# Optimization experiments

Measured on AMD Instinct MI355X. Metric: run time of the kernel, lower is better.

## Reference

```python
import jax, jax.numpy as jnp
import numpy as np

H = 16      # query heads
G = 4       # kv heads
D = 64      # head dim
ROPE_BASE = 10000.0

def _rotate_half(t):
    t1, t2 = jnp.split(t, 2, axis=-1)
    return jnp.concatenate([-t2, t1], axis=-1)

def _rope_emb(n):
    inv_freq = 1.0 / (ROPE_BASE ** (jnp.arange(0, D, 2, dtype=jnp.float32) / D))
    freqs = jnp.outer(jnp.arange(n, dtype=jnp.float32), inv_freq)  # [n, D/2]
    return jnp.concatenate([freqs, freqs], axis=-1)               # [n, D]

def setup_inputs() -> dict:
    key = jax.random.key(0)
    k1, k2, k3, k4 = jax.random.split(key, 4)
    B, N, C = 2, 2048, 1024
    x = jax.random.normal(k1, (B, N, C), dtype=jnp.float32)
    w_q = jax.random.normal(k2, (C, C), dtype=jnp.float32) * 0.02
    w_kv = jax.random.normal(k3, (C, 2 * G * D), dtype=jnp.float32) * 0.02
    w_out = jax.random.normal(k4, (C, C), dtype=jnp.float32) * 0.02
    return {"x": x, "w_q": w_q, "w_kv": w_kv, "w_out": w_out}

def reference(x, w_q, w_kv, w_out):
    B, N, C = x.shape
    scale = D ** -0.5
    q = (x @ w_q).reshape(B, N, H, D).transpose(0, 2, 1, 3)        # [B,H,N,D]
    kv = x @ w_kv
    k, v = jnp.split(kv, 2, axis=-1)
    k = k.reshape(B, N, G, D).transpose(0, 2, 1, 3)                # [B,G,N,D]
    v = v.reshape(B, N, G, D).transpose(0, 2, 1, 3)
    emb = _rope_emb(N)                                             # [N,D]
    cos, sin = jnp.cos(emb), jnp.sin(emb)
    q = q * cos + _rotate_half(q) * sin
    k = k * cos + _rotate_half(k) * sin
    # NOTE: faithful to source einsum -- kv-head axis g is SUMMED (absent from output)
    scores = jnp.einsum('bhid,bgjd->bhij', q, k) * scale           # [B,H,N,N]
    probs = jax.nn.softmax(scores, axis=-1)
    out = jnp.einsum('bhij,bgjd->bhid', probs, v)                  # [B,H,N,D]
    out = out.transpose(0, 2, 1, 3).reshape(B, N, H * D)
    return out @ w_out
```

## Files before the change

### kernel.cpp

```cpp
#include <hip/hip_runtime.h>
#include <hip/hip_bf16.h>
#include <math.h>

#define B_ 2
#define N_ 2048
#define C_ 1024
#define H_ 16
#define G_ 4
#define D_ 64

using short8  = __attribute__((ext_vector_type(8))) short;
using float4v = __attribute__((ext_vector_type(4))) float;

__device__ __forceinline__ ushort f2bf(float f) {
    union { float f; unsigned u; } v; v.f = f;
    unsigned r = (v.u + 0x7FFF + ((v.u >> 16) & 1)) >> 16;
    return (ushort)r;
}
__device__ __forceinline__ float bf2f(ushort u) {
    union { unsigned u; float f; } t; t.u = ((unsigned)u) << 16; return t.f;
}
__device__ __forceinline__ unsigned pack_bf16(float a, float b) {
#if __has_builtin(__builtin_amdgcn_cvt_pk_bf16_f32)
    auto t = __builtin_amdgcn_cvt_pk_bf16_f32(a, b);
    unsigned r; __builtin_memcpy(&r, &t, 4); return r;
#else
    return (unsigned)f2bf(a) | ((unsigned)f2bf(b) << 16);
#endif
}
__device__ __forceinline__ float fexp2(float x) {
#if __has_builtin(__builtin_amdgcn_exp2f)
    return __builtin_amdgcn_exp2f(x);
#else
    return exp2f(x);
#endif
}

__global__ void convert_x(const float* __restrict__ x, ushort* __restrict__ xb) {
    int i = (blockIdx.x * 256 + threadIdx.x) * 4;
    float4 v = *(const float4*)(x + i);
    ushort4 o;
    o.x = f2bf(v.x); o.y = f2bf(v.y); o.z = f2bf(v.z); o.w = f2bf(v.w);
    *(ushort4*)(xb + i) = o;
}

__global__ void tconv(const float* __restrict__ src, ushort* __restrict__ dst,
                      int K, int N) {
    __shared__ float T[64][65];
    const int n0 = blockIdx.x * 64, k0 = blockIdx.y * 64;
    const int tid = threadIdx.x;
    #pragma unroll
    for (int s = 0; s < 16; ++s) {
        int idx = tid + s * 256; int r = idx >> 6, cc = idx & 63;
        T[r][cc] = src[(size_t)(k0 + r) * N + n0 + cc];
    }
    __syncthreads();
    #pragma unroll
    for (int s = 0; s < 16; ++s) {
        int idx = tid + s * 256; int r = idx >> 6, cc = idx & 63;
        dst[(size_t)(n0 + r) * K + k0 + cc] = f2bf(T[cc][r]);
    }
}

template <bool F32OUT>
__global__ __launch_bounds__(256) void gemm64(const ushort* __restrict__ A,
                                              const ushort* __restrict__ Bt,
                                              void* __restrict__ Cv,
                                              int M, int N, int K) {
    __shared__ __align__(16) ushort As[64 * 32];
    __shared__ __align__(16) ushort Bs[64 * 32];

    const int tid = threadIdx.x, wave = tid >> 6, lane = tid & 63;
    const int g = lane >> 4, c = lane & 15;
    const int wr = wave >> 1, wc = wave & 1;
    const int m0 = blockIdx.y * 64, n0 = blockIdx.x * 64;

    const int srow = wave * 16 + (lane >> 2), schunk = (lane & 3) * 8;
    const ushort* pa = A  + (size_t)(m0 + srow) * K + schunk;
    const ushort* pb = Bt + (size_t)(n0 + srow) * K + schunk;
    ushort* ldsA = &As[wave * 16 * 32];
    ushort* ldsB = &Bs[wave * 16 * 32];

    float4v acc[2][2] = {{{0,0,0,0},{0,0,0,0}},{{0,0,0,0},{0,0,0,0}}};

    for (int k0 = 0; k0 < K; k0 += 32) {
        __builtin_amdgcn_global_load_lds(
            (const __attribute__((address_space(1))) void*)(pa + k0),
            (__attribute__((address_space(3))) void*)ldsA, 16, 0, 0);
        __builtin_amdgcn_global_load_lds(
            (const __attribute__((address_space(1))) void*)(pb + k0),
            (__attribute__((address_space(3))) void*)ldsB, 16, 0, 0);
        __syncthreads();

        short8 af0 = *(const short8*)&As[(wr * 32 + c) * 32 + 8 * g];
        short8 af1 = *(const short8*)&As[(wr * 32 + 16 + c) * 32 + 8 * g];
        short8 bf0 = *(const short8*)&Bs[(wc * 32 + c) * 32 + 8 * g];
        short8 bf1 = *(const short8*)&Bs[(wc * 32 + 16 + c) * 32 + 8 * g];
        acc[0][0] = __builtin_amdgcn_mfma_f32_16x16x32_bf16(af0, bf0, acc[0][0], 0, 0, 0);
        acc[0][1] = __builtin_amdgcn_mfma_f32_16x16x32_bf16(af0, bf1, acc[0][1], 0, 0, 0);
        acc[1][0] = __builtin_amdgcn_mfma_f32_16x16x32_bf16(af1, bf0, acc[1][0], 0, 0, 0);
        acc[1][1] = __builtin_amdgcn_mfma_f32_16x16x32_bf16(af1, bf1, acc[1][1], 0, 0, 0);
        __syncthreads();
    }

    #pragma unroll
    for (int a = 0; a < 2; ++a)
        #pragma unroll
        for (int bb = 0; bb < 2; ++bb)
            #pragma unroll
            for (int r = 0; r < 4; ++r) {
                int rowi = m0 + wr * 32 + a * 16 + 4 * g + r;
                int coli = n0 + wc * 32 + bb * 16 + c;
                if (F32OUT) ((float*)Cv)[(size_t)rowi * N + coli] = acc[a][bb][r];
                else ((ushort*)Cv)[(size_t)rowi * N + coli] = f2bf(acc[a][bb][r]);
            }
}

__global__ void kv_reduce2(const ushort* __restrict__ qkvb,
                           ushort* __restrict__ Kt, ushort* __restrict__ VtT) {
    const int wid = threadIdx.x >> 6, d = threadIdx.x & 63;
    const int rowg = blockIdx.x * 4 + wid;
    const int n = rowg & (N_ - 1), b = rowg >> 11;

    const ushort* base = qkvb + (size_t)rowg * 1536 + 1024;
    float ks = 0.f, vs = 0.f;
    #pragma unroll
    for (int g = 0; g < G_; ++g) {
        ks += bf2f(base[g * 64 + d]);
        vs += bf2f(base[256 + g * 64 + d]);
    }
    float partner = __shfl_xor(ks, 32, 64);
    float rh = (d < 32) ? -partner : partner;
    float ang = (float)n * __powf(10000.0f, -(float)(d & 31) * (1.0f / 32.0f));
    float sn, cs; __sincosf(ang, &sn, &cs);

    Kt[(size_t)rowg * 64 + d] = f2bf(ks * cs + rh * sn);
    int jp = (n & ~31) | (((n & 15) << 1) | ((n >> 4) & 1));
    VtT[((size_t)b * 64 + d) * N_ + jp] = f2bf(vs);
}

#define PS 40
#define QSCALE 0.18033688011112042f

__global__ __launch_bounds__(256) void attn5(
        const ushort* __restrict__ qkvb, const ushort* __restrict__ Kt,
        const ushort* __restrict__ VtT,
        ushort* __restrict__ oP0, ushort* __restrict__ oP1,
        float* __restrict__ lP0, float* __restrict__ lP1) {
    const int s  = blockIdx.x & 1;
    const int qt = (blockIdx.x >> 1) & 7;
    const int h  = (blockIdx.x >> 4) & 15;
    const int b  = blockIdx.x >> 8;
    const int tid = threadIdx.x, wave = tid >> 6, lane = tid & 63;
    const int g = lane >> 4, c = lane & 15;

    __shared__ __align__(16) ushort Ksh[64 * 64];
    __shared__ __align__(16) ushort Vsh[64 * 64];
    __shared__ __align__(16) ushort Psh[4][64 * PS];

    ushort* oPs = s ? oP1 : oP0;
    float*  lPs = s ? lP1 : lP0;

    const int i0 = qt * 256 + wave * 64;
    short8 qf[4][2];
    #pragma unroll
    for (int a = 0; a < 4; ++a) {
        const int row = i0 + a * 16 + c;
        const ushort* qrow = qkvb + (size_t)(b * N_ + row) * 1536 + h * 64;
        short8 raw0 = *(const short8*)(qrow + 8 * g);
        short8 raw1 = *(const short8*)(qrow + 32 + 8 * g);
        #pragma unroll
        for (int i = 0; i < 8; ++i) {
            int dd = 8 * g + i;
            float f0 = bf2f((ushort)raw0[i]), f1 = bf2f((ushort)raw1[i]);
            float ang = (float)row * __powf(10000.0f, -(float)dd * (1.0f / 32.0f));
            float sn, cs; __sincosf(ang, &sn, &cs);
            qf[a][0][i] = (short)f2bf((f0 * cs - f1 * sn) * QSCALE);
            qf[a][1][i] = (short)f2bf((f1 * cs + f0 * sn) * QSCALE);
        }
    }

    const short8 ones = {(short)0x3F80, (short)0x3F80, (short)0x3F80, (short)0x3F80,
                         (short)0x3F80, (short)0x3F80, (short)0x3F80, (short)0x3F80};

    float4v o[4][4];
    float4v o4[4];
    #pragma unroll
    for (int a = 0; a < 4; ++a) {
        o4[a] = {0, 0, 0, 0};
        #pragma unroll
        for (int f = 0; f < 4; ++f) o[a][f] = {0, 0, 0, 0};
    }

    const ushort* Kb = Kt  + (size_t)b * N_ * 64;
    const ushort* Vb = VtT + (size_t)b * 64 * N_;
    const int lr8 = lane >> 3, lq8 = lane & 7;
    const int swz = (lq8 ^ lr8) * 8;
    const int j0 = s * (N_ / 2);

    for (int jt = j0; jt < j0 + N_ / 2; jt += 64) {
        __syncthreads();
        #pragma unroll
        for (int t = 0; t < 2; ++t) {
            const int row8 = wave * 16 + t * 8;
            __builtin_amdgcn_global_load_lds(
                (const __attribute__((address_space(1))) void*)
                    (Kb + (size_t)(jt + row8 + lr8) * 64 + swz),
                (__attribute__((address_space(3))) void*)&Ksh[row8 * 64], 16, 0, 0);
            __builtin_amdgcn_global_load_lds(
                (const __attribute__((address_space(1))) void*)
                    (Vb + (size_t)(row8 + lr8) * N_ + jt + swz),
                (__attribute__((address_space(3))) void*)&Vsh[row8 * 64], 16, 0, 0);
        }
        __syncthreads();

        #pragma unroll
        for (int jj = 0; jj < 64; jj += 32) {
            float4v sc[4][2];
            #pragma unroll
            for (int t = 0; t < 2; ++t) {
                const int R = jj + 16 * t + c;
                short8 ka = *(const short8*)&Ksh[R * 64 + ((g ^ (c & 7)) * 8)];
                short8 kb = *(const short8*)&Ksh[R * 64 + (((g ^ 4) ^ (c & 7)) * 8)];
                #pragma unroll
                for (int a = 0; a < 4; ++a) {
                    if (t == 0) { sc[a][0] = {0,0,0,0}; sc[a][1] = {0,0,0,0}; }
                    sc[a][t] = __builtin_amdgcn_mfma_f32_16x16x32_bf16(qf[a][0], ka, sc[a][t], 0, 0, 0);
                    sc[a][t] = __builtin_amdgcn_mfma_f32_16x16x32_bf16(qf[a][1], kb, sc[a][t], 0, 0, 0);
                }
            }
            #pragma unroll
            for (int a = 0; a < 4; ++a)
                #pragma unroll
                for (int r = 0; r < 4; ++r) {
                    float p0 = fexp2(sc[a][0][r]), p1 = fexp2(sc[a][1][r]);
                    ((unsigned*)&Psh[wave][(a * 16 + 4 * g + r) * PS])[c] = pack_bf16(p0, p1);
                }
            const int vb = (jj >> 3);
            #pragma unroll
            for (int a = 0; a < 4; ++a) {
                short8 pf = *(const short8*)&Psh[wave][(a * 16 + c) * PS + 8 * g];
                #pragma unroll
                for (int f = 0; f < 4; ++f) {
                    const int R = 16 * f + c;
                    short8 vf = *(const short8*)&Vsh[R * 64 + (((g ^ vb) ^ (c & 7)) * 8)];
                    o[a][f] = __builtin_amdgcn_mfma_f32_16x16x32_bf16(pf, vf, o[a][f], 0, 0, 0);
                }
                o4[a] = __builtin_amdgcn_mfma_f32_16x16x32_bf16(pf, ones, o4[a], 0, 0, 0);
            }
        }
    }

    #pragma unroll
    for (int a = 0; a < 4; ++a)
        #pragma unroll
        for (int r = 0; r < 4; ++r) {
            const int row = i0 + a * 16 + 4 * g + r;
            if (c == 0) lPs[(size_t)(b * N_ + row) * 16 + h] = o4[a][r];
            size_t base = (size_t)(b * N_ + row) * 1024 + h * 64 + c;
            oPs[base]      = f2bf(o[a][0][r]);
            oPs[base + 16] = f2bf(o[a][1][r]);
            oPs[base + 32] = f2bf(o[a][2][r]);
            oPs[base + 48] = f2bf(o[a][3][r]);
        }
}

__global__ void combine(const ushort* __restrict__ oP0, const ushort* __restrict__ oP1,
                        const float* __restrict__ lP0, const float* __restrict__ lP1,
                        ushort* __restrict__ ao) {
    const int e = (blockIdx.x * 256 + threadIdx.x) * 4;
    const int row = e >> 10, hh = (e >> 6) & 15;
    const float inv = 1.0f / (lP0[row * 16 + hh] + lP1[row * 16 + hh]);
    ushort4 a = *(const ushort4*)(oP0 + e);
    ushort4 b = *(const ushort4*)(oP1 + e);
    ushort4 r;
    r.x = f2bf((bf2f(a.x) + bf2f(b.x)) * inv);
    r.y = f2bf((bf2f(a.y) + bf2f(b.y)) * inv);
    r.z = f2bf((bf2f(a.z) + bf2f(b.z)) * inv);
    r.w = f2bf((bf2f(a.w) + bf2f(b.w)) * inv);
    *(ushort4*)(ao + e) = r;
}

extern "C" void kernel_launch(void* const* d_in, const int* in_sizes, int n_in,
                              void* d_out, int out_size, void* d_ws, size_t ws_size,
                              hipStream_t stream) {
    const float* x     = (const float*)d_in[0];
    const float* w_q   = (const float*)d_in[1];
    const float* w_kv  = (const float*)d_in[2];
    const float* w_out = (const float*)d_in[3];
    float* out = (float*)d_out;

    const int M = B_ * N_;
    ushort* xb    = (ushort*)d_ws;
    ushort* wqkvT = xb    + (size_t)M * C_;
    ushort* woutT = wqkvT + (size_t)1536 * C_;
    ushort* qkvb  = woutT + (size_t)C_ * C_;
    ushort* Kt    = qkvb  + (size_t)M * 1536;
    ushort* VtT   = Kt    + (size_t)B_ * N_ * D_;
    ushort* oP1   = VtT   + (size_t)B_ * D_ * N_;
    float*  lP0   = (float*)(oP1 + (size_t)M * C_);
    float*  lP1   = lP0 + (size_t)M * H_;
    ushort* oP0   = xb;
    ushort* ao    = xb;

    convert_x<<<(M * C_) / 1024, 256, 0, stream>>>(x, xb);
    tconv<<<dim3(16, 16), 256, 0, stream>>>(w_q,  wqkvT,                   C_, C_);
    tconv<<<dim3(8, 16),  256, 0, stream>>>(w_kv, wqkvT + (size_t)C_ * C_, C_, 2 * G_ * D_);
    tconv<<<dim3(16, 16), 256, 0, stream>>>(w_out, woutT,                  C_, C_);

    gemm64<false><<<dim3(1536 / 64, M / 64), 256, 0, stream>>>(xb, wqkvT, qkvb, M, 1536, C_);
    kv_reduce2<<<M / 4, 256, 0, stream>>>(qkvb, Kt, VtT);
    attn5<<<B_ * H_ * (N_ / 256) * 2, 256, 0, stream>>>(qkvb, Kt, VtT, oP0, oP1, lP0, lP1);
    combine<<<(M * C_) / 1024, 256, 0, stream>>>(oP0, oP1, lP0, lP1, ao);
    gemm64<true><<<dim3(C_ / 64, M / 64), 256, 0, stream>>>(ao, woutT, out, M, C_, C_);
}
```

Before: 200.5 us.

## Double-buffer K/V tiles in attention and enlarge GEMM tiles to 128x64

The attention kernel now uses two LDS buffers for K and V, issuing the load for the next tile before computing on the current one, with one barrier per iteration instead of two. The P scratch buffer shrinks to one 16-row slab per wave that is reused for each row group. Both projection GEMMs move from 64x64 to 128x64 block tiles so each wave computes 32x64 and B fragments are reused across more MFMAs. This trades more LDS and registers per block, and so possibly lower occupancy, for hidden load latency and better data reuse.

```diff
diff --git a/kernel.cpp b/kernel.cpp
--- a/kernel.cpp
+++ b/kernel.cpp
@@ -63,56 +63,64 @@
 }
 
 template <bool F32OUT>
-__global__ __launch_bounds__(256) void gemm64(const ushort* __restrict__ A,
-                                              const ushort* __restrict__ Bt,
-                                              void* __restrict__ Cv,
-                                              int M, int N, int K) {
-    __shared__ __align__(16) ushort As[64 * 32];
+__global__ __launch_bounds__(256) void gemm128x64(const ushort* __restrict__ A,
+                                                  const ushort* __restrict__ Bt,
+                                                  void* __restrict__ Cv,
+                                                  int M, int N, int K) {
+    __shared__ __align__(16) ushort As[128 * 32];
     __shared__ __align__(16) ushort Bs[64 * 32];
 
     const int tid = threadIdx.x, wave = tid >> 6, lane = tid & 63;
     const int g = lane >> 4, c = lane & 15;
-    const int wr = wave >> 1, wc = wave & 1;
-    const int m0 = blockIdx.y * 64, n0 = blockIdx.x * 64;
-
-    const int srow = wave * 16 + (lane >> 2), schunk = (lane & 3) * 8;
-    const ushort* pa = A  + (size_t)(m0 + srow) * K + schunk;
-    const ushort* pb = Bt + (size_t)(n0 + srow) * K + schunk;
-    ushort* ldsA = &As[wave * 16 * 32];
-    ushort* ldsB = &Bs[wave * 16 * 32];
-
-    float4v acc[2][2] = {{{0,0,0,0},{0,0,0,0}},{{0,0,0,0},{0,0,0,0}}};
+    const int m0 = blockIdx.y * 128, n0 = blockIdx.x * 64;
+
+    const int srow = lane >> 2, schunk = (lane & 3) * 8;
+    const ushort* paA0 = A  + (size_t)(m0 + wave * 32 + srow) * K + schunk;
+    const ushort* paA1 = A  + (size_t)(m0 + wave * 32 + 16 + srow) * K + schunk;
+    const ushort* paB  = Bt + (size_t)(n0 + wave * 16 + srow) * K + schunk;
+    ushort* ldsA0 = &As[(wave * 32) * 32];
+    ushort* ldsA1 = &As[(wave * 32 + 16) * 32];
+    ushort* ldsB  = &Bs[(wave * 16) * 32];
+
+    float4v acc[2][4];
+    #pragma unroll
+    for (int a = 0; a < 2; ++a)
+        #pragma unroll
+        for (int n = 0; n < 4; ++n) acc[a][n] = {0, 0, 0, 0};
 
     for (int k0 = 0; k0 < K; k0 += 32) {
         __builtin_amdgcn_global_load_lds(
-            (const __attribute__((address_space(1))) void*)(pa + k0),
-            (__attribute__((address_space(3))) void*)ldsA, 16, 0, 0);
+            (const __attribute__((address_space(1))) void*)(paA0 + k0),
+            (__attribute__((address_space(3))) void*)ldsA0, 16, 0, 0);
         __builtin_amdgcn_global_load_lds(
-            (const __attribute__((address_space(1))) void*)(pb + k0),
+            (const __attribute__((address_space(1))) void*)(paA1 + k0),
+            (__attribute__((address_space(3))) void*)ldsA1, 16, 0, 0);
+        __builtin_amdgcn_global_load_lds(
+            (const __attribute__((address_space(1))) void*)(paB + k0),
             (__attribute__((address_space(3))) void*)ldsB, 16, 0, 0);
         __syncthreads();
 
-        short8 af0 = *(const short8*)&As[(wr * 32 + c) * 32 + 8 * g];
-        short8 af1 = *(const short8*)&As[(wr * 32 + 16 + c) * 32 + 8 * g];
-        short8 bf0 = *(const short8*)&Bs[(wc * 32 + c) * 32 + 8 * g];
-        short8 bf1 = *(const short8*)&Bs[(wc * 32 + 16 + c) * 32 + 8 * g];
-        acc[0][0] = __builtin_amdgcn_mfma_f32_16x16x32_bf16(af0, bf0, acc[0][0], 0, 0, 0);
-        acc[0][1] = __builtin_amdgcn_mfma_f32_16x16x32_bf16(af0, bf1, acc[0][1], 0, 0, 0);
-        acc[1][0] = __builtin_amdgcn_mfma_f32_16x16x32_bf16(af1, bf0, acc[1][0], 0, 0, 0);
-        acc[1][1] = __builtin_amdgcn_mfma_f32_16x16x32_bf16(af1, bf1, acc[1][1], 0, 0, 0);
+        short8 af0 = *(const short8*)&As[(wave * 32 + c) * 32 + 8 * g];
+        short8 af1 = *(const short8*)&As[(wave * 32 + 16 + c) * 32 + 8 * g];
+        #pragma unroll
+        for (int n = 0; n < 4; ++n) {
+            short8 bfn = *(const short8*)&Bs[(n * 16 + c) * 32 + 8 * g];
+            acc[0][n] = __builtin_amdgcn_mfma_f32_16x16x32_bf16(af0, bfn, acc[0][n], 0, 0, 0);
+            acc[1][n] = __builtin_amdgcn_mfma_f32_16x16x32_bf16(af1, bfn, acc[1][n], 0, 0, 0);
+        }
         __syncthreads();
     }
 
     #pragma unroll
     for (int a = 0; a < 2; ++a)
         #pragma unroll
-        for (int bb = 0; bb < 2; ++bb)
+        for (int n = 0; n < 4; ++n)
             #pragma unroll
             for (int r = 0; r < 4; ++r) {
-                int rowi = m0 + wr * 32 + a * 16 + 4 * g + r;
-                int coli = n0 + wc * 32 + bb * 16 + c;
-                if (F32OUT) ((float*)Cv)[(size_t)rowi * N + coli] = acc[a][bb][r];
-                else ((ushort*)Cv)[(size_t)rowi * N + coli] = f2bf(acc[a][bb][r]);
+                int rowi = m0 + wave * 32 + a * 16 + 4 * g + r;
+                int coli = n0 + n * 16 + c;
+                if (F32OUT) ((float*)Cv)[(size_t)rowi * N + coli] = acc[a][n][r];
+                else ((ushort*)Cv)[(size_t)rowi * N + coli] = f2bf(acc[a][n][r]);
             }
 }
 
@@ -142,7 +150,7 @@
 #define PS 40
 #define QSCALE 0.18033688011112042f
 
-__global__ __launch_bounds__(256) void attn5(
+__global__ __launch_bounds__(256) void attn6(
         const ushort* __restrict__ qkvb, const ushort* __restrict__ Kt,
         const ushort* __restrict__ VtT,
         ushort* __restrict__ oP0, ushort* __restrict__ oP1,
@@ -154,9 +162,9 @@
     const int tid = threadIdx.x, wave = tid >> 6, lane = tid & 63;
     const int g = lane >> 4, c = lane & 15;
 
-    __shared__ __align__(16) ushort Ksh[64 * 64];
-    __shared__ __align__(16) ushort Vsh[64 * 64];
-    __shared__ __align__(16) ushort Psh[4][64 * PS];
+    __shared__ __align__(16) ushort Ksh[2][64 * 64];
+    __shared__ __align__(16) ushort Vsh[2][64 * 64];
+    __shared__ __align__(16) ushort Psh[4][16 * PS];
 
     ushort* oPs = s ? oP1 : oP0;
     float*  lPs = s ? lP1 : lP0;
@@ -197,53 +205,59 @@
     const int lr8 = lane >> 3, lq8 = lane & 7;
     const int swz = (lq8 ^ lr8) * 8;
     const int j0 = s * (N_ / 2);
-
-    for (int jt = j0; jt < j0 + N_ / 2; jt += 64) {
-        __syncthreads();
+    const int NT = (N_ / 2) / 64;
+
+    auto stage = [&](int j, int bi) {
         #pragma unroll
         for (int t = 0; t < 2; ++t) {
             const int row8 = wave * 16 + t * 8;
             __builtin_amdgcn_global_load_lds(
                 (const __attribute__((address_space(1))) void*)
-                    (Kb + (size_t)(jt + row8 + lr8) * 64 + swz),
-                (__attribute__((address_space(3))) void*)&Ksh[row8 * 64], 16, 0, 0);
+                    (Kb + (size_t)(j + row8 + lr8) * 64 + swz),
+                (__attribute__((address_space(3))) void*)&Ksh[bi][row8 * 64], 16, 0, 0);
             __builtin_amdgcn_global_load_lds(
                 (const __attribute__((address_space(1))) void*)
-                    (Vb + (size_t)(row8 + lr8) * N_ + jt + swz),
-                (__attribute__((address_space(3))) void*)&Vsh[row8 * 64], 16, 0, 0);
-        }
+                    (Vb + (size_t)(row8 + lr8) * N_ + j + swz),
+                (__attribute__((address_space(3))) void*)&Vsh[bi][row8 * 64], 16, 0, 0);
+        }
+    };
+
+    stage(j0, 0);
+
+    for (int t = 0; t < NT; ++t) {
         __syncthreads();
+        if (t + 1 < NT) stage(j0 + (t + 1) * 64, (t + 1) & 1);
+        const ushort* Kc = Ksh[t & 1];
+        const ushort* Vc = Vsh[t & 1];
 
         #pragma unroll
         for (int jj = 0; jj < 64; jj += 32) {
             float4v sc[4][2];
             #pragma unroll
-            for (int t = 0; t < 2; ++t) {
-                const int R = jj + 16 * t + c;
-                short8 ka = *(const short8*)&Ksh[R * 64 + ((g ^ (c & 7)) * 8)];
-                short8 kb = *(const short8*)&Ksh[R * 64 + (((g ^ 4) ^ (c & 7)) * 8)];
+            for (int tt = 0; tt < 2; ++tt) {
+                const int R = jj + 16 * tt + c;
+                short8 ka = *(const short8*)&Kc[R * 64 + ((g ^ (c & 7)) * 8)];
+                short8 kb = *(const short8*)&Kc[R * 64 + (((g ^ 4) ^ (c & 7)) * 8)];
                 #pragma unroll
                 for (int a = 0; a < 4; ++a) {
-                    if (t == 0) { sc[a][0] = {0,0,0,0}; sc[a][1] = {0,0,0,0}; }
-                    sc[a][t] = __builtin_amdgcn_mfma_f32_16x16x32_bf16(qf[a][0], ka, sc[a][t], 0, 0, 0);
-                    sc[a][t] = __builtin_amdgcn_mfma_f32_16x16x32_bf16(qf[a][1], kb, sc[a][t], 0, 0, 0);
+                    if (tt == 0) { sc[a][0] = {0,0,0,0}; sc[a][1] = {0,0,0,0}; }
+                    sc[a][tt] = __builtin_amdgcn_mfma_f32_16x16x32_bf16(qf[a][0], ka, sc[a][tt], 0, 0, 0);
+                    sc[a][tt] = __builtin_amdgcn_mfma_f32_16x16x32_bf16(qf[a][1], kb, sc[a][tt], 0, 0, 0);
                 }
             }
+            const int vb = (jj >> 3);
             #pragma unroll
-            for (int a = 0; a < 4; ++a)
+            for (int a = 0; a < 4; ++a) {
                 #pragma unroll
                 for (int r = 0; r < 4; ++r) {
                     float p0 = fexp2(sc[a][0][r]), p1 = fexp2(sc[a][1][r]);
-                    ((unsigned*)&Psh[wave][(a * 16 + 4 * g + r) * PS])[c] = pack_bf16(p0, p1);
+                    ((unsigned*)&Psh[wave][(4 * g + r) * PS])[c] = pack_bf16(p0, p1);
                 }
-            const int vb = (jj >> 3);
-            #pragma unroll
-            for (int a = 0; a < 4; ++a) {
-                short8 pf = *(const short8*)&Psh[wave][(a * 16 + c) * PS + 8 * g];
+                short8 pf = *(const short8*)&Psh[wave][c * PS + 8 * g];
                 #pragma unroll
                 for (int f = 0; f < 4; ++f) {
                     const int R = 16 * f + c;
-                    short8 vf = *(const short8*)&Vsh[R * 64 + (((g ^ vb) ^ (c & 7)) * 8)];
+                    short8 vf = *(const short8*)&Vc[R * 64 + (((g ^ vb) ^ (c & 7)) * 8)];
                     o[a][f] = __builtin_amdgcn_mfma_f32_16x16x32_bf16(pf, vf, o[a][f], 0, 0, 0);
                 }
                 o4[a] = __builtin_amdgcn_mfma_f32_16x16x32_bf16(pf, ones, o4[a], 0, 0, 0);
@@ -308,9 +322,9 @@
     tconv<<<dim3(8, 16),  256, 0, stream>>>(w_kv, wqkvT + (size_t)C_ * C_, C_, 2 * G_ * D_);
     tconv<<<dim3(16, 16), 256, 0, stream>>>(w_out, woutT,                  C_, C_);
 
-    gemm64<false><<<dim3(1536 / 64, M / 64), 256, 0, stream>>>(xb, wqkvT, qkvb, M, 1536, C_);
+    gemm128x64<false><<<dim3(1536 / 64, M / 128), 256, 0, stream>>>(xb, wqkvT, qkvb, M, 1536, C_);
     kv_reduce2<<<M / 4, 256, 0, stream>>>(qkvb, Kt, VtT);
-    attn5<<<B_ * H_ * (N_ / 256) * 2, 256, 0, stream>>>(qkvb, Kt, VtT, oP0, oP1, lP0, lP1);
+    attn6<<<B_ * H_ * (N_ / 256) * 2, 256, 0, stream>>>(qkvb, Kt, VtT, oP0, oP1, lP0, lP1);
     combine<<<(M * C_) / 1024, 256, 0, stream>>>(oP0, oP1, lP0, lP1, ao);
-    gemm64<true><<<dim3(C_ / 64, M / 64), 256, 0, stream>>>(ao, woutT, out, M, C_, C_);
-}
+    gemm128x64<true><<<dim3(C_ / 64, M / 128), 256, 0, stream>>>(ao, woutT, out, M, C_, C_);
+}
```

New measurement: 226.3 us. 1.13x slower.

## Compute transposed scores to keep P in registers; prefetch K/V; deepen GEMM k-tile

Applied to the files above, without the earlier changes.

The attention kernel now computes S^T (K as the A operand), so each lane's score results already match the B-operand layout of a 16x16x16 bf16 MFMA for PV. This removes the LDS round-trip for P and the extra ones-MFMA used for the row sums, which are now accumulated in registers and reduced with shuffles. K/V tiles are register-prefetched one iteration ahead and stored to swizzled LDS, replacing the direct global-to-LDS loads. The GEMM k-step grows from 32 to 64, halving barriers per iteration at the cost of more LDS. PV now uses more, smaller MFMA instructions.

```diff
diff --git a/kernel.cpp b/kernel.cpp
--- a/kernel.cpp
+++ b/kernel.cpp
@@ -10,7 +10,14 @@
 #define D_ 64
 
 using short8  = __attribute__((ext_vector_type(8))) short;
+using short4v = __attribute__((ext_vector_type(4))) short;
 using float4v = __attribute__((ext_vector_type(4))) float;
+
+#if __has_builtin(__builtin_amdgcn_mfma_f32_16x16x16_bf16)
+#define MFMA16K16(A, B, C) __builtin_amdgcn_mfma_f32_16x16x16_bf16(A, B, C, 0, 0, 0)
+#else
+#define MFMA16K16(A, B, C) __builtin_amdgcn_mfma_f32_16x16x16bf16_1k(A, B, C, 0, 0, 0)
+#endif
 
 __device__ __forceinline__ ushort f2bf(float f) {
     union { float f; unsigned u; } v; v.f = f;
@@ -67,39 +74,43 @@
                                               const ushort* __restrict__ Bt,
                                               void* __restrict__ Cv,
                                               int M, int N, int K) {
-    __shared__ __align__(16) ushort As[64 * 32];
-    __shared__ __align__(16) ushort Bs[64 * 32];
+    __shared__ __align__(16) ushort As[64 * 64];
+    __shared__ __align__(16) ushort Bs[64 * 64];
 
     const int tid = threadIdx.x, wave = tid >> 6, lane = tid & 63;
     const int g = lane >> 4, c = lane & 15;
     const int wr = wave >> 1, wc = wave & 1;
     const int m0 = blockIdx.y * 64, n0 = blockIdx.x * 64;
 
-    const int srow = wave * 16 + (lane >> 2), schunk = (lane & 3) * 8;
-    const ushort* pa = A  + (size_t)(m0 + srow) * K + schunk;
-    const ushort* pb = Bt + (size_t)(n0 + srow) * K + schunk;
-    ushort* ldsA = &As[wave * 16 * 32];
-    ushort* ldsB = &Bs[wave * 16 * 32];
+    const int srow = lane >> 3, schunk = (lane & 7) * 8;
+    const ushort* pa = A  + (size_t)(m0 + wave * 16 + srow) * K + schunk;
+    const ushort* pb = Bt + (size_t)(n0 + wave * 16 + srow) * K + schunk;
 
     float4v acc[2][2] = {{{0,0,0,0},{0,0,0,0}},{{0,0,0,0},{0,0,0,0}}};
 
-    for (int k0 = 0; k0 < K; k0 += 32) {
-        __builtin_amdgcn_global_load_lds(
-            (const __attribute__((address_space(1))) void*)(pa + k0),
-            (__attribute__((address_space(3))) void*)ldsA, 16, 0, 0);
-        __builtin_amdgcn_global_load_lds(
-            (const __attribute__((address_space(1))) void*)(pb + k0),
-            (__attribute__((address_space(3))) void*)ldsB, 16, 0, 0);
+    for (int k0 = 0; k0 < K; k0 += 64) {
+        #pragma unroll
+        for (int t = 0; t < 2; ++t) {
+            __builtin_amdgcn_global_load_lds(
+                (const __attribute__((address_space(1))) void*)(pa + (size_t)t * 8 * K + k0),
+                (__attribute__((address_space(3))) void*)&As[(wave * 16 + t * 8) * 64], 16, 0, 0);
+            __builtin_amdgcn_global_load_lds(
+                (const __attribute__((address_space(1))) void*)(pb + (size_t)t * 8 * K + k0),
+                (__attribute__((address_space(3))) void*)&Bs[(wave * 16 + t * 8) * 64], 16, 0, 0);
+        }
         __syncthreads();
 
-        short8 af0 = *(const short8*)&As[(wr * 32 + c) * 32 + 8 * g];
-        short8 af1 = *(const short8*)&As[(wr * 32 + 16 + c) * 32 + 8 * g];
-        short8 bf0 = *(const short8*)&Bs[(wc * 32 + c) * 32 + 8 * g];
-        short8 bf1 = *(const short8*)&Bs[(wc * 32 + 16 + c) * 32 + 8 * g];
-        acc[0][0] = __builtin_amdgcn_mfma_f32_16x16x32_bf16(af0, bf0, acc[0][0], 0, 0, 0);
-        acc[0][1] = __builtin_amdgcn_mfma_f32_16x16x32_bf16(af0, bf1, acc[0][1], 0, 0, 0);
-        acc[1][0] = __builtin_amdgcn_mfma_f32_16x16x32_bf16(af1, bf0, acc[1][0], 0, 0, 0);
-        acc[1][1] = __builtin_amdgcn_mfma_f32_16x16x32_bf16(af1, bf1, acc[1][1], 0, 0, 0);
+        #pragma unroll
+        for (int kk = 0; kk < 2; ++kk) {
+            short8 af0 = *(const short8*)&As[(wr * 32 + c) * 64 + kk * 32 + 8 * g];
+            short8 af1 = *(const short8*)&As[(wr * 32 + 16 + c) * 64 + kk * 32 + 8 * g];
+            short8 bf0 = *(const short8*)&Bs[(wc * 32 + c) * 64 + kk * 32 + 8 * g];
+            short8 bf1 = *(const short8*)&Bs[(wc * 32 + 16 + c) * 64 + kk * 32 + 8 * g];
+            acc[0][0] = __builtin_amdgcn_mfma_f32_16x16x32_bf16(af0, bf0, acc[0][0], 0, 0, 0);
+            acc[0][1] = __builtin_amdgcn_mfma_f32_16x16x32_bf16(af0, bf1, acc[0][1], 0, 0, 0);
+            acc[1][0] = __builtin_amdgcn_mfma_f32_16x16x32_bf16(af1, bf0, acc[1][0], 0, 0, 0);
+            acc[1][1] = __builtin_amdgcn_mfma_f32_16x16x32_bf16(af1, bf1, acc[1][1], 0, 0, 0);
+        }
         __syncthreads();
     }
 
@@ -135,14 +146,12 @@
     float sn, cs; __sincosf(ang, &sn, &cs);
 
     Kt[(size_t)rowg * 64 + d] = f2bf(ks * cs + rh * sn);
-    int jp = (n & ~31) | (((n & 15) << 1) | ((n >> 4) & 1));
-    VtT[((size_t)b * 64 + d) * N_ + jp] = f2bf(vs);
-}
-
-#define PS 40
+    VtT[((size_t)b * 64 + d) * N_ + n] = f2bf(vs);
+}
+
 #define QSCALE 0.18033688011112042f
 
-__global__ __launch_bounds__(256) void attn5(
+__global__ __launch_bounds__(256) void attn7(
         const ushort* __restrict__ qkvb, const ushort* __restrict__ Kt,
         const ushort* __restrict__ VtT,
         ushort* __restrict__ oP0, ushort* __restrict__ oP1,
@@ -156,7 +165,6 @@
 
     __shared__ __align__(16) ushort Ksh[64 * 64];
     __shared__ __align__(16) ushort Vsh[64 * 64];
-    __shared__ __align__(16) ushort Psh[4][64 * PS];
 
     ushort* oPs = s ? oP1 : oP0;
     float*  lPs = s ? lP1 : lP0;
@@ -180,89 +188,84 @@
         }
     }
 
-    const short8 ones = {(short)0x3F80, (short)0x3F80, (short)0x3F80, (short)0x3F80,
-                         (short)0x3F80, (short)0x3F80, (short)0x3F80, (short)0x3F80};
-
     float4v o[4][4];
-    float4v o4[4];
-    #pragma unroll
-    for (int a = 0; a < 4; ++a) {
-        o4[a] = {0, 0, 0, 0};
+    #pragma unroll
+    for (int a = 0; a < 4; ++a)
         #pragma unroll
         for (int f = 0; f < 4; ++f) o[a][f] = {0, 0, 0, 0};
-    }
+    float ll[4] = {0.f, 0.f, 0.f, 0.f};
 
     const ushort* Kb = Kt  + (size_t)b * N_ * 64;
     const ushort* Vb = VtT + (size_t)b * 64 * N_;
     const int lr8 = lane >> 3, lq8 = lane & 7;
-    const int swz = (lq8 ^ lr8) * 8;
+    const int wpos = (lq8 ^ lr8) * 8;
     const int j0 = s * (N_ / 2);
-
-    for (int jt = j0; jt < j0 + N_ / 2; jt += 64) {
+    const int NT = (N_ / 2) / 64;
+
+    short8 kr0 = *(const short8*)(Kb + (size_t)(j0 + wave * 16 + lr8) * 64 + lq8 * 8);
+    short8 kr1 = *(const short8*)(Kb + (size_t)(j0 + wave * 16 + 8 + lr8) * 64 + lq8 * 8);
+    short8 vr0 = *(const short8*)(Vb + (size_t)(wave * 16 + lr8) * N_ + j0 + lq8 * 8);
+    short8 vr1 = *(const short8*)(Vb + (size_t)(wave * 16 + 8 + lr8) * N_ + j0 + lq8 * 8);
+
+    for (int t = 0; t < NT; ++t) {
         __syncthreads();
-        #pragma unroll
-        for (int t = 0; t < 2; ++t) {
-            const int row8 = wave * 16 + t * 8;
-            __builtin_amdgcn_global_load_lds(
-                (const __attribute__((address_space(1))) void*)
-                    (Kb + (size_t)(jt + row8 + lr8) * 64 + swz),
-                (__attribute__((address_space(3))) void*)&Ksh[row8 * 64], 16, 0, 0);
-            __builtin_amdgcn_global_load_lds(
-                (const __attribute__((address_space(1))) void*)
-                    (Vb + (size_t)(row8 + lr8) * N_ + jt + swz),
-                (__attribute__((address_space(3))) void*)&Vsh[row8 * 64], 16, 0, 0);
-        }
+        *(short8*)&Ksh[(wave * 16 + lr8) * 64 + wpos]     = kr0;
+        *(short8*)&Ksh[(wave * 16 + 8 + lr8) * 64 + wpos] = kr1;
+        *(short8*)&Vsh[(wave * 16 + lr8) * 64 + wpos]     = vr0;
+        *(short8*)&Vsh[(wave * 16 + 8 + lr8) * 64 + wpos] = vr1;
         __syncthreads();
-
-        #pragma unroll
-        for (int jj = 0; jj < 64; jj += 32) {
-            float4v sc[4][2];
+        if (t + 1 < NT) {
+            const int jn = j0 + (t + 1) * 64;
+            kr0 = *(const short8*)(Kb + (size_t)(jn + wave * 16 + lr8) * 64 + lq8 * 8);
+            kr1 = *(const short8*)(Kb + (size_t)(jn + wave * 16 + 8 + lr8) * 64 + lq8 * 8);
+            vr0 = *(const short8*)(Vb + (size_t)(wave * 16 + lr8) * N_ + jn + lq8 * 8);
+            vr1 = *(const short8*)(Vb + (size_t)(wave * 16 + 8 + lr8) * N_ + jn + lq8 * 8);
+        }
+
+        #pragma unroll
+        for (int jt4 = 0; jt4 < 4; ++jt4) {
+            const int R = jt4 * 16 + c;
+            short8 kf0 = *(const short8*)&Ksh[R * 64 + ((g ^ (c & 7)) * 8)];
+            short8 kf1 = *(const short8*)&Ksh[R * 64 + (((g ^ 4) ^ (c & 7)) * 8)];
+            short4v vf[4];
             #pragma unroll
-            for (int t = 0; t < 2; ++t) {
-                const int R = jj + 16 * t + c;
-                short8 ka = *(const short8*)&Ksh[R * 64 + ((g ^ (c & 7)) * 8)];
-                short8 kb = *(const short8*)&Ksh[R * 64 + (((g ^ 4) ^ (c & 7)) * 8)];
-                #pragma unroll
-                for (int a = 0; a < 4; ++a) {
-                    if (t == 0) { sc[a][0] = {0,0,0,0}; sc[a][1] = {0,0,0,0}; }
-                    sc[a][t] = __builtin_amdgcn_mfma_f32_16x16x32_bf16(qf[a][0], ka, sc[a][t], 0, 0, 0);
-                    sc[a][t] = __builtin_amdgcn_mfma_f32_16x16x32_bf16(qf[a][1], kb, sc[a][t], 0, 0, 0);
-                }
-            }
-            #pragma unroll
-            for (int a = 0; a < 4; ++a)
-                #pragma unroll
-                for (int r = 0; r < 4; ++r) {
-                    float p0 = fexp2(sc[a][0][r]), p1 = fexp2(sc[a][1][r]);
-                    ((unsigned*)&Psh[wave][(a * 16 + 4 * g + r) * PS])[c] = pack_bf16(p0, p1);
-                }
-            const int vb = (jj >> 3);
+            for (int f = 0; f < 4; ++f)
+                vf[f] = *(const short4v*)&Vsh[(16 * f + c) * 64 +
+                          (((jt4 * 2 + (g >> 1)) ^ (c & 7)) * 8) + (g & 1) * 4];
+
             #pragma unroll
             for (int a = 0; a < 4; ++a) {
-                short8 pf = *(const short8*)&Psh[wave][(a * 16 + c) * PS + 8 * g];
+                float4v st = {0, 0, 0, 0};
+                st = __builtin_amdgcn_mfma_f32_16x16x32_bf16(kf0, qf[a][0], st, 0, 0, 0);
+                st = __builtin_amdgcn_mfma_f32_16x16x32_bf16(kf1, qf[a][1], st, 0, 0, 0);
+                float p0 = fexp2(st[0]), p1 = fexp2(st[1]);
+                float p2 = fexp2(st[2]), p3 = fexp2(st[3]);
+                ll[a] += (p0 + p1) + (p2 + p3);
+                union { unsigned u[2]; short4v v; } pk;
+                pk.u[0] = pack_bf16(p0, p1);
+                pk.u[1] = pack_bf16(p2, p3);
                 #pragma unroll
-                for (int f = 0; f < 4; ++f) {
-                    const int R = 16 * f + c;
-                    short8 vf = *(const short8*)&Vsh[R * 64 + (((g ^ vb) ^ (c & 7)) * 8)];
-                    o[a][f] = __builtin_amdgcn_mfma_f32_16x16x32_bf16(pf, vf, o[a][f], 0, 0, 0);
-                }
-                o4[a] = __builtin_amdgcn_mfma_f32_16x16x32_bf16(pf, ones, o4[a], 0, 0, 0);
+                for (int f = 0; f < 4; ++f)
+                    o[a][f] = MFMA16K16(vf[f], pk.v, o[a][f]);
             }
         }
     }
 
     #pragma unroll
-    for (int a = 0; a < 4; ++a)
-        #pragma unroll
-        for (int r = 0; r < 4; ++r) {
-            const int row = i0 + a * 16 + 4 * g + r;
-            if (c == 0) lPs[(size_t)(b * N_ + row) * 16 + h] = o4[a][r];
-            size_t base = (size_t)(b * N_ + row) * 1024 + h * 64 + c;
-            oPs[base]      = f2bf(o[a][0][r]);
-            oPs[base + 16] = f2bf(o[a][1][r]);
-            oPs[base + 32] = f2bf(o[a][2][r]);
-            oPs[base + 48] = f2bf(o[a][3][r]);
-        }
+    for (int a = 0; a < 4; ++a) {
+        float lt = ll[a];
+        lt += __shfl_xor(lt, 16, 64);
+        lt += __shfl_xor(lt, 32, 64);
+        const int row = i0 + a * 16 + c;
+        if (g == 0) lPs[(size_t)(b * N_ + row) * 16 + h] = lt;
+        #pragma unroll
+        for (int f = 0; f < 4; ++f) {
+            ushort4 w;
+            w.x = f2bf(o[a][f][0]); w.y = f2bf(o[a][f][1]);
+            w.z = f2bf(o[a][f][2]); w.w = f2bf(o[a][f][3]);
+            *(ushort4*)(oPs + (size_t)(b * N_ + row) * 1024 + h * 64 + 16 * f + 4 * g) = w;
+        }
+    }
 }
 
 __global__ void combine(const ushort* __restrict__ oP0, const ushort* __restrict__ oP1,
@@ -310,7 +313,7 @@
 
     gemm64<false><<<dim3(1536 / 64, M / 64), 256, 0, stream>>>(xb, wqkvT, qkvb, M, 1536, C_);
     kv_reduce2<<<M / 4, 256, 0, stream>>>(qkvb, Kt, VtT);
-    attn5<<<B_ * H_ * (N_ / 256) * 2, 256, 0, stream>>>(qkvb, Kt, VtT, oP0, oP1, lP0, lP1);
+    attn7<<<B_ * H_ * (N_ / 256) * 2, 256, 0, stream>>>(qkvb, Kt, VtT, oP0, oP1, lP0, lP1);
     combine<<<(M * C_) / 1024, 256, 0, stream>>>(oP0, oP1, lP0, lP1, ao);
     gemm64<true><<<dim3(C_ / 64, M / 64), 256, 0, stream>>>(ao, woutT, out, M, C_, C_);
 }
```

Result: no change. 196.8 us (-1.9%).
